# Performance work log

Hardware: AMD Instinct MI355X
Metric: run time of the kernel (lower is better)

The kernel has to match this reference:

```python
import jax, jax.numpy as jnp
import numpy as np
import math

D = 64          # emb_size
R = 32          # num relations
MAX_LEN = 5000  # position table size
E = 30000       # num edges / relation instances
EPSILON = 0.01
THETA = 0.01


def _build_Q():
    # sinusoidal axes [MAX_LEN, D]
    position = jnp.arange(MAX_LEN, dtype=jnp.float32)[:, None]
    div_term = jnp.exp(jnp.arange(0, D, 2, dtype=jnp.float32) * (-math.log(10000.0) / D))
    axes = jnp.zeros((MAX_LEN, D), dtype=jnp.float32)
    axes = axes.at[:, 0::2].set(jnp.sin(position * div_term))
    axes = axes.at[:, 1::2].set(jnp.cos(position * div_term))
    # skew-symmetric generator S_ij = theta * (a_i - a_j); Q = expm(S)  [MAX_LEN, D, D]
    S = THETA * (axes[..., None] - axes[:, None, :])
    Q = jax.scipy.linalg.expm(S)
    return Q


def setup_inputs() -> dict:
    key = jax.random.key(0)
    k1, k2, k3, k4, k5 = jax.random.split(key, 5)
    std = 1.0 / jnp.sqrt(jnp.float32(D))
    relation_embs = jax.random.normal(k1, (R, D, D), dtype=jnp.float32) * std
    Q = _build_Q()
    relation_mapping = jax.random.randint(k2, (E, 2), 0, 2 * R, dtype=jnp.int64 if jax.config.jax_enable_x64 else jnp.int32)
    node_mapping = jax.random.randint(k3, (MAX_LEN,), 0, MAX_LEN)
    edge_index = jax.random.randint(k4, (2, E), 0, MAX_LEN)
    node_embs = jax.random.normal(k5, (MAX_LEN, D), dtype=jnp.float32)
    return {
        "relation_mapping": relation_mapping,
        "node_mapping": node_mapping,
        "edge_index": edge_index,
        "node_embs": node_embs,
        "relation_embs": relation_embs,
        "Q": Q,
    }


def reference(relation_mapping, node_mapping, edge_index, node_embs, relation_embs, Q):
    # node_mapping, edge_index, node_embs are unused by the original forward
    I = jnp.eye(D, dtype=relation_embs.dtype)
    W_even = I + EPSILON * relation_embs   # [R, D, D]
    W_odd = I - EPSILON * relation_embs    # [R, D, D]
    # interleave -> W[2r] = W_even[r], W[2r+1] = W_odd[r]   [2R, D, D]
    W = jnp.stack([W_even, W_odd], axis=1).reshape(-1, D, D)
    Qg = Q[relation_mapping[:, 0]]         # [E, D, D] gather
    rel = W[relation_mapping[:, 1]]        # [E, D, D] gather
    # Q^T @ rel @ Q per edge
    out = jnp.einsum('eji,ejk,ekl->eil', Qg, rel, Qg)
    return out  # dropout p=0.0 is identity
```

## Files before the change

kernel.cpp:

```cpp
#include <hip/hip_runtime.h>

#define TRE_EPS 0.01f
#define TRE_CAP 256
#define TRE_NB  2048

typedef float tre_f4 __attribute__((ext_vector_type(4)));
typedef short tre_bf8 __attribute__((ext_vector_type(8)));

__device__ __forceinline__ unsigned short tre_f2bf(float f) {
    unsigned int u = __float_as_uint(f);
    u += 0x7fffu + ((u >> 16) & 1u);
    return (unsigned short)(u >> 16);
}
__device__ __forceinline__ unsigned long long tre_pack4(float a, float b,
                                                        float c, float d) {
    return (unsigned long long)tre_f2bf(a)
         | ((unsigned long long)tre_f2bf(b) << 16)
         | ((unsigned long long)tre_f2bf(c) << 32)
         | ((unsigned long long)tre_f2bf(d) << 48);
}

__global__ __launch_bounds__(256) void tre_bin(
    const int* __restrict__ rm, int E,
    int* __restrict__ counts, int* __restrict__ list)
{
    int e = blockIdx.x * 256 + threadIdx.x;
    if (e >= E) return;
    int g  = rm[2 * e + 0];
    int r2 = rm[2 * e + 1];
    int b  = (g << 5) | (r2 >> 1);
    int idx = atomicAdd(&counts[b], 1);
    if (idx < TRE_CAP)
        list[b * TRE_CAP + idx] = (e << 1) | (r2 & 1);
}

__global__ __launch_bounds__(256) void tre_pair(
    const float* __restrict__ Q, const float* __restrict__ RE,
    const int* __restrict__ counts, const int* __restrict__ list,
    float* __restrict__ out)
{
    __shared__ __align__(16) unsigned char sB[16384];
    __shared__ int sList[TRE_CAP];

    const int b = blockIdx.x;
    const int g = b >> 5;
    const int r = b & 31;
    const int t = threadIdx.x;
    const int lane = t & 63;
    const int wv = t >> 6;
    const int fr = lane & 15;
    const int fq = lane >> 4;
    const int i0 = wv << 4;

    const int cnt_raw = counts[b];
    const int cnt = cnt_raw > TRE_CAP ? TRE_CAP : cnt_raw;
    if (t < cnt) sList[t] = list[b * TRE_CAP + t];

    const float* Qg  = Q  + ((size_t)g << 12);
    const float* REr = RE + ((size_t)r << 12);

    unsigned char* REb = sB;
    unsigned char* Qtb = sB + 8192;

    for (int i = t; i < 1024; i += 256) {
        float4 w = ((const float4*)REr)[i];
        int R = i >> 4, c0 = (i & 15) << 2;
        int o = c0 * 2;
        *(unsigned long long*)(REb + R * 128 + (o ^ ((R & 7) << 4))) =
            tre_pack4(w.x, w.y, w.z, w.w);
    }
    for (int it = 0; it < 4; ++it) {
        int k0 = (wv << 2) + (it << 4);
        float q0 = Qg[(k0 + 0) * 64 + lane];
        float q1 = Qg[(k0 + 1) * 64 + lane];
        float q2 = Qg[(k0 + 2) * 64 + lane];
        float q3 = Qg[(k0 + 3) * 64 + lane];
        int R = lane, o = k0 * 2;
        *(unsigned long long*)(Qtb + R * 128 + (o ^ ((R & 7) << 4))) =
            tre_pack4(q0, q1, q2, q3);
    }
    __syncthreads();

    tre_f4 accA[4];
#pragma unroll
    for (int jf = 0; jf < 4; ++jf) accA[jf] = (tre_f4){0.f, 0.f, 0.f, 0.f};
#pragma unroll
    for (int ks = 0; ks < 2; ++ks) {
        int ko = ks * 64 + fq * 16;
        int Ra = i0 + fr;
        tre_bf8 afr = *(const tre_bf8*)(REb + Ra * 128 + (ko ^ ((Ra & 7) << 4)));
#pragma unroll
        for (int jf = 0; jf < 4; ++jf) {
            int Rb = (jf << 4) + fr;
            tre_bf8 bfr = *(const tre_bf8*)(Qtb + Rb * 128 + (ko ^ ((Rb & 7) << 4)));
            accA[jf] = __builtin_amdgcn_mfma_f32_16x16x32_bf16(afr, bfr, accA[jf], 0, 0, 0);
        }
    }
    __syncthreads();

#pragma unroll
    for (int jf = 0; jf < 4; ++jf) {
        int C  = (jf << 4) + fr;
        int r0 = i0 + (fq << 2);
        int o  = r0 * 2;
        *(unsigned long long*)(sB + C * 128 + (o ^ ((C & 7) << 4))) =
            tre_pack4(accA[jf][0], accA[jf][1], accA[jf][2], accA[jf][3]);
    }
    __syncthreads();

    tre_f4 accM[4];
#pragma unroll
    for (int jf = 0; jf < 4; ++jf) accM[jf] = (tre_f4){0.f, 0.f, 0.f, 0.f};
#pragma unroll
    for (int ks = 0; ks < 2; ++ks) {
        int ko = ks * 64 + fq * 16;
        int Ra = i0 + fr;
        tre_bf8 afr = *(const tre_bf8*)(Qtb + Ra * 128 + (ko ^ ((Ra & 7) << 4)));
#pragma unroll
        for (int jf = 0; jf < 4; ++jf) {
            int Rb = (jf << 4) + fr;
            tre_bf8 bfr = *(const tre_bf8*)(sB + Rb * 128 + (ko ^ ((Rb & 7) << 4)));
            accM[jf] = __builtin_amdgcn_mfma_f32_16x16x32_bf16(afr, bfr, accM[jf], 0, 0, 0);
        }
    }
    __syncthreads();

    float* sM = (float*)sB;
#pragma unroll
    for (int jf = 0; jf < 4; ++jf) {
        int c  = (jf << 4) + fr;
        int r0 = i0 + (fq << 2);
        sM[(r0 + 0) * 64 + c] = accM[jf][0];
        sM[(r0 + 1) * 64 + c] = accM[jf][1];
        sM[(r0 + 2) * 64 + c] = accM[jf][2];
        sM[(r0 + 3) * 64 + c] = accM[jf][3];
    }
    __syncthreads();

    tre_f4 mreg[4], diag[4];
#pragma unroll
    for (int j = 0; j < 4; ++j) {
        mreg[j] = *(const tre_f4*)&sM[(t + 256 * j) << 2];
        int f = (t + 256 * j) << 2;
#pragma unroll
        for (int c = 0; c < 4; ++c) {
            int fc = f + c;
            diag[j][c] = ((fc >> 6) == (fc & 63)) ? 1.0f : 0.0f;
        }
    }

    if (cnt > 0) {
        int pk = sList[0];
        for (int i = 0; i < cnt; ++i) {
            int nxt = (i + 1 < cnt) ? sList[i + 1] : 0;
            int e = pk >> 1;
            float s = (pk & 1) ? -TRE_EPS : TRE_EPS;
            tre_f4* dst = (tre_f4*)(out + ((size_t)e << 12));
#pragma unroll
            for (int j = 0; j < 4; ++j) {
                tre_f4 v = s * mreg[j] + diag[j];
                __builtin_nontemporal_store(v, &dst[t + 256 * j]);
            }
            pk = nxt;
        }
    }
}

__global__ __launch_bounds__(256) void tre_direct(
    const int* __restrict__ rm, const float* __restrict__ Q,
    const float* __restrict__ RE, float* __restrict__ out)
{
    __shared__ float sQ[64 * 64];
    __shared__ float sW[64 * 65];

    const int e = blockIdx.x;
    const int g  = rm[2 * e + 0];
    const int r2 = rm[2 * e + 1];
    const int r  = r2 >> 1;
    const float s = (r2 & 1) ? -TRE_EPS : TRE_EPS;
    const int t = threadIdx.x;
    const int i0 = (t >> 4) << 2;
    const int l0 = (t & 15) << 2;

    const float* Qg  = Q  + ((size_t)g << 12);
    const float* REr = RE + ((size_t)r << 12);
    for (int i = t; i < 1024; i += 256) {
        ((float4*)sQ)[i] = ((const float4*)Qg)[i];
        float4 w = ((const float4*)REr)[i];
        int row = i >> 4, col = (i & 15) << 2;
        float* dst = &sW[row * 65 + col];
        dst[0] = w.x; dst[1] = w.y; dst[2] = w.z; dst[3] = w.w;
    }
    __syncthreads();

    float a[4][4] = {{0,0,0,0},{0,0,0,0},{0,0,0,0},{0,0,0,0}};
#pragma unroll 8
    for (int k = 0; k < 64; ++k) {
        float4 qv = *(const float4*)&sQ[(k << 6) + l0];
#pragma unroll
        for (int d = 0; d < 4; ++d) {
            float w = sW[(i0 + d) * 65 + k];
            a[d][0] = fmaf(w, qv.x, a[d][0]);
            a[d][1] = fmaf(w, qv.y, a[d][1]);
            a[d][2] = fmaf(w, qv.z, a[d][2]);
            a[d][3] = fmaf(w, qv.w, a[d][3]);
        }
    }
    __syncthreads();
    float* sA = sW;
#pragma unroll
    for (int d = 0; d < 4; ++d)
        *(float4*)&sA[(i0 + d) * 64 + l0] =
            make_float4(a[d][0], a[d][1], a[d][2], a[d][3]);
    __syncthreads();

    float qtq[4][4] = {{0,0,0,0},{0,0,0,0},{0,0,0,0},{0,0,0,0}};
    float qta[4][4] = {{0,0,0,0},{0,0,0,0},{0,0,0,0},{0,0,0,0}};
#pragma unroll 4
    for (int j = 0; j < 64; ++j) {
        float4 qi = *(const float4*)&sQ[(j << 6) + i0];
        float4 ql = *(const float4*)&sQ[(j << 6) + l0];
        float4 av = *(const float4*)&sA[(j << 6) + l0];
        float qiv[4] = {qi.x, qi.y, qi.z, qi.w};
        float qlv[4] = {ql.x, ql.y, ql.z, ql.w};
        float avv[4] = {av.x, av.y, av.z, av.w};
#pragma unroll
        for (int d = 0; d < 4; ++d)
#pragma unroll
            for (int ee = 0; ee < 4; ++ee) {
                qtq[d][ee] = fmaf(qiv[d], qlv[ee], qtq[d][ee]);
                qta[d][ee] = fmaf(qiv[d], avv[ee], qta[d][ee]);
            }
    }
    float* dst = out + ((size_t)e << 12);
#pragma unroll
    for (int d = 0; d < 4; ++d) {
        float4 v;
        v.x = fmaf(s, qta[d][0], qtq[d][0]);
        v.y = fmaf(s, qta[d][1], qtq[d][1]);
        v.z = fmaf(s, qta[d][2], qtq[d][2]);
        v.w = fmaf(s, qta[d][3], qtq[d][3]);
        *(float4*)&dst[(i0 + d) * 64 + l0] = v;
    }
}

extern "C" void kernel_launch(void* const* d_in, const int* in_sizes, int n_in,
                              void* d_out, int out_size, void* d_ws, size_t ws_size,
                              hipStream_t stream) {
    const int*   rm = (const int*)d_in[0];
    const float* RE = (const float*)d_in[4];
    const float* Q  = (const float*)d_in[5];
    float* out = (float*)d_out;
    const int E = in_sizes[0] / 2;

    const size_t cnt_bytes  = (size_t)TRE_NB * sizeof(int);
    const size_t list_bytes = (size_t)TRE_NB * TRE_CAP * sizeof(int);
    const size_t need = cnt_bytes + list_bytes;

    if (ws_size >= need) {
        int* counts = (int*)d_ws;
        int* list   = (int*)((char*)d_ws + cnt_bytes);
        hipMemsetAsync(counts, 0, cnt_bytes, stream);
        hipLaunchKernelGGL(tre_bin, dim3((E + 255) / 256), dim3(256), 0, stream,
                           rm, E, counts, list);
        hipLaunchKernelGGL(tre_pair, dim3(TRE_NB), dim3(256), 0, stream,
                           Q, RE, counts, list, out);
    } else {
        hipLaunchKernelGGL(tre_direct, dim3(E), dim3(256), 0, stream,
                           rm, Q, RE, out);
    }
}
```

Measured before the change: 116.1 us.

## Make pair kernel persistent with atomic work-stealing over bins

Turns the per-bin pair kernel into a persistent kernel launched with a fixed grid. Each block takes further bins from a global atomic cursor, which tre_bin initialises. Empty bins are skipped before any Q/RE loads, and load imbalance from uneven bin counts should even out through dynamic scheduling. In exchange it adds an atomic and two barriers per bin and serialises bins within a block.

```diff
diff --git a/kernel.cpp b/kernel.cpp
--- a/kernel.cpp
+++ b/kernel.cpp
@@ -1,8 +1,9 @@
 #include <hip/hip_runtime.h>
 
-#define TRE_EPS 0.01f
-#define TRE_CAP 256
-#define TRE_NB  2048
+#define TRE_EPS   0.01f
+#define TRE_CAP   256
+#define TRE_NB    2048
+#define TRE_PGRID 1024
 
 typedef float tre_f4 __attribute__((ext_vector_type(4)));
 typedef short tre_bf8 __attribute__((ext_vector_type(8)));
@@ -22,8 +23,9 @@
 
 __global__ __launch_bounds__(256) void tre_bin(
     const int* __restrict__ rm, int E,
-    int* __restrict__ counts, int* __restrict__ list)
+    int* __restrict__ counts, int* __restrict__ list, int* __restrict__ cursor)
 {
+    if (blockIdx.x == 0 && threadIdx.x == 0) *cursor = TRE_PGRID;
     int e = blockIdx.x * 256 + threadIdx.x;
     if (e >= E) return;
     int g  = rm[2 * e + 0];
@@ -34,17 +36,15 @@
         list[b * TRE_CAP + idx] = (e << 1) | (r2 & 1);
 }
 
-__global__ __launch_bounds__(256) void tre_pair(
+__global__ __launch_bounds__(256, 4) void tre_pair(
     const float* __restrict__ Q, const float* __restrict__ RE,
     const int* __restrict__ counts, const int* __restrict__ list,
-    float* __restrict__ out)
+    int* __restrict__ cursor, float* __restrict__ out)
 {
     __shared__ __align__(16) unsigned char sB[16384];
     __shared__ int sList[TRE_CAP];
-
-    const int b = blockIdx.x;
-    const int g = b >> 5;
-    const int r = b & 31;
+    __shared__ int sTicket;
+
     const int t = threadIdx.x;
     const int lane = t & 63;
     const int wv = t >> 6;
@@ -52,95 +52,12 @@
     const int fq = lane >> 4;
     const int i0 = wv << 4;
 
-    const int cnt_raw = counts[b];
-    const int cnt = cnt_raw > TRE_CAP ? TRE_CAP : cnt_raw;
-    if (t < cnt) sList[t] = list[b * TRE_CAP + t];
-
-    const float* Qg  = Q  + ((size_t)g << 12);
-    const float* REr = RE + ((size_t)r << 12);
-
     unsigned char* REb = sB;
     unsigned char* Qtb = sB + 8192;
 
-    for (int i = t; i < 1024; i += 256) {
-        float4 w = ((const float4*)REr)[i];
-        int R = i >> 4, c0 = (i & 15) << 2;
-        int o = c0 * 2;
-        *(unsigned long long*)(REb + R * 128 + (o ^ ((R & 7) << 4))) =
-            tre_pack4(w.x, w.y, w.z, w.w);
-    }
-    for (int it = 0; it < 4; ++it) {
-        int k0 = (wv << 2) + (it << 4);
-        float q0 = Qg[(k0 + 0) * 64 + lane];
-        float q1 = Qg[(k0 + 1) * 64 + lane];
-        float q2 = Qg[(k0 + 2) * 64 + lane];
-        float q3 = Qg[(k0 + 3) * 64 + lane];
-        int R = lane, o = k0 * 2;
-        *(unsigned long long*)(Qtb + R * 128 + (o ^ ((R & 7) << 4))) =
-            tre_pack4(q0, q1, q2, q3);
-    }
-    __syncthreads();
-
-    tre_f4 accA[4];
-#pragma unroll
-    for (int jf = 0; jf < 4; ++jf) accA[jf] = (tre_f4){0.f, 0.f, 0.f, 0.f};
-#pragma unroll
-    for (int ks = 0; ks < 2; ++ks) {
-        int ko = ks * 64 + fq * 16;
-        int Ra = i0 + fr;
-        tre_bf8 afr = *(const tre_bf8*)(REb + Ra * 128 + (ko ^ ((Ra & 7) << 4)));
-#pragma unroll
-        for (int jf = 0; jf < 4; ++jf) {
-            int Rb = (jf << 4) + fr;
-            tre_bf8 bfr = *(const tre_bf8*)(Qtb + Rb * 128 + (ko ^ ((Rb & 7) << 4)));
-            accA[jf] = __builtin_amdgcn_mfma_f32_16x16x32_bf16(afr, bfr, accA[jf], 0, 0, 0);
-        }
-    }
-    __syncthreads();
-
-#pragma unroll
-    for (int jf = 0; jf < 4; ++jf) {
-        int C  = (jf << 4) + fr;
-        int r0 = i0 + (fq << 2);
-        int o  = r0 * 2;
-        *(unsigned long long*)(sB + C * 128 + (o ^ ((C & 7) << 4))) =
-            tre_pack4(accA[jf][0], accA[jf][1], accA[jf][2], accA[jf][3]);
-    }
-    __syncthreads();
-
-    tre_f4 accM[4];
-#pragma unroll
-    for (int jf = 0; jf < 4; ++jf) accM[jf] = (tre_f4){0.f, 0.f, 0.f, 0.f};
-#pragma unroll
-    for (int ks = 0; ks < 2; ++ks) {
-        int ko = ks * 64 + fq * 16;
-        int Ra = i0 + fr;
-        tre_bf8 afr = *(const tre_bf8*)(Qtb + Ra * 128 + (ko ^ ((Ra & 7) << 4)));
-#pragma unroll
-        for (int jf = 0; jf < 4; ++jf) {
-            int Rb = (jf << 4) + fr;
-            tre_bf8 bfr = *(const tre_bf8*)(sB + Rb * 128 + (ko ^ ((Rb & 7) << 4)));
-            accM[jf] = __builtin_amdgcn_mfma_f32_16x16x32_bf16(afr, bfr, accM[jf], 0, 0, 0);
-        }
-    }
-    __syncthreads();
-
-    float* sM = (float*)sB;
-#pragma unroll
-    for (int jf = 0; jf < 4; ++jf) {
-        int c  = (jf << 4) + fr;
-        int r0 = i0 + (fq << 2);
-        sM[(r0 + 0) * 64 + c] = accM[jf][0];
-        sM[(r0 + 1) * 64 + c] = accM[jf][1];
-        sM[(r0 + 2) * 64 + c] = accM[jf][2];
-        sM[(r0 + 3) * 64 + c] = accM[jf][3];
-    }
-    __syncthreads();
-
-    tre_f4 mreg[4], diag[4];
+    tre_f4 diag[4];
 #pragma unroll
     for (int j = 0; j < 4; ++j) {
-        mreg[j] = *(const tre_f4*)&sM[(t + 256 * j) << 2];
         int f = (t + 256 * j) << 2;
 #pragma unroll
         for (int c = 0; c < 4; ++c) {
@@ -149,20 +66,120 @@
         }
     }
 
-    if (cnt > 0) {
-        int pk = sList[0];
-        for (int i = 0; i < cnt; ++i) {
-            int nxt = (i + 1 < cnt) ? sList[i + 1] : 0;
-            int e = pk >> 1;
-            float s = (pk & 1) ? -TRE_EPS : TRE_EPS;
-            tre_f4* dst = (tre_f4*)(out + ((size_t)e << 12));
-#pragma unroll
-            for (int j = 0; j < 4; ++j) {
-                tre_f4 v = s * mreg[j] + diag[j];
-                __builtin_nontemporal_store(v, &dst[t + 256 * j]);
-            }
-            pk = nxt;
+    int b = blockIdx.x;
+    for (;;) {
+        if (b >= TRE_NB) break;
+
+        const int cnt_raw = counts[b];
+        const int cnt = cnt_raw > TRE_CAP ? TRE_CAP : cnt_raw;
+
+        if (cnt > 0) {
+            const int g = b >> 5;
+            const int r = b & 31;
+            const float* Qg  = Q  + ((size_t)g << 12);
+            const float* REr = RE + ((size_t)r << 12);
+
+            if (t < cnt) sList[t] = list[b * TRE_CAP + t];
+
+            for (int i = t; i < 1024; i += 256) {
+                float4 w = ((const float4*)REr)[i];
+                int R = i >> 4, c0 = (i & 15) << 2;
+                int o = c0 * 2;
+                *(unsigned long long*)(REb + R * 128 + (o ^ ((R & 7) << 4))) =
+                    tre_pack4(w.x, w.y, w.z, w.w);
+            }
+            for (int it = 0; it < 4; ++it) {
+                int k0 = (wv << 2) + (it << 4);
+                float q0 = Qg[(k0 + 0) * 64 + lane];
+                float q1 = Qg[(k0 + 1) * 64 + lane];
+                float q2 = Qg[(k0 + 2) * 64 + lane];
+                float q3 = Qg[(k0 + 3) * 64 + lane];
+                int R = lane, o = k0 * 2;
+                *(unsigned long long*)(Qtb + R * 128 + (o ^ ((R & 7) << 4))) =
+                    tre_pack4(q0, q1, q2, q3);
+            }
+            __syncthreads();
+
+            tre_f4 accA[4];
+#pragma unroll
+            for (int jf = 0; jf < 4; ++jf) accA[jf] = (tre_f4){0.f, 0.f, 0.f, 0.f};
+#pragma unroll
+            for (int ks = 0; ks < 2; ++ks) {
+                int ko = ks * 64 + fq * 16;
+                int Ra = i0 + fr;
+                tre_bf8 afr = *(const tre_bf8*)(REb + Ra * 128 + (ko ^ ((Ra & 7) << 4)));
+#pragma unroll
+                for (int jf = 0; jf < 4; ++jf) {
+                    int Rb = (jf << 4) + fr;
+                    tre_bf8 bfr = *(const tre_bf8*)(Qtb + Rb * 128 + (ko ^ ((Rb & 7) << 4)));
+                    accA[jf] = __builtin_amdgcn_mfma_f32_16x16x32_bf16(afr, bfr, accA[jf], 0, 0, 0);
+                }
+            }
+            __syncthreads();
+
+#pragma unroll
+            for (int jf = 0; jf < 4; ++jf) {
+                int C  = (jf << 4) + fr;
+                int r0 = i0 + (fq << 2);
+                int o  = r0 * 2;
+                *(unsigned long long*)(sB + C * 128 + (o ^ ((C & 7) << 4))) =
+                    tre_pack4(accA[jf][0], accA[jf][1], accA[jf][2], accA[jf][3]);
+            }
+            __syncthreads();
+
+            tre_f4 accM[4];
+#pragma unroll
+            for (int jf = 0; jf < 4; ++jf) accM[jf] = (tre_f4){0.f, 0.f, 0.f, 0.f};
+#pragma unroll
+            for (int ks = 0; ks < 2; ++ks) {
+                int ko = ks * 64 + fq * 16;
+                int Ra = i0 + fr;
+                tre_bf8 afr = *(const tre_bf8*)(Qtb + Ra * 128 + (ko ^ ((Ra & 7) << 4)));
+#pragma unroll
+                for (int jf = 0; jf < 4; ++jf) {
+                    int Rb = (jf << 4) + fr;
+                    tre_bf8 bfr = *(const tre_bf8*)(sB + Rb * 128 + (ko ^ ((Rb & 7) << 4)));
+                    accM[jf] = __builtin_amdgcn_mfma_f32_16x16x32_bf16(afr, bfr, accM[jf], 0, 0, 0);
+                }
+            }
+            __syncthreads();
+
+            float* sM = (float*)sB;
+#pragma unroll
+            for (int jf = 0; jf < 4; ++jf) {
+                int cc = (jf << 4) + fr;
+                int r0 = i0 + (fq << 2);
+                sM[(r0 + 0) * 64 + cc] = accM[jf][0];
+                sM[(r0 + 1) * 64 + cc] = accM[jf][1];
+                sM[(r0 + 2) * 64 + cc] = accM[jf][2];
+                sM[(r0 + 3) * 64 + cc] = accM[jf][3];
+            }
+            __syncthreads();
+
+            tre_f4 mreg[4];
+#pragma unroll
+            for (int j = 0; j < 4; ++j)
+                mreg[j] = *(const tre_f4*)&sM[(t + 256 * j) << 2];
+
+            int pk = sList[0];
+            for (int i = 0; i < cnt; ++i) {
+                int nxt = (i + 1 < cnt) ? sList[i + 1] : 0;
+                int e = pk >> 1;
+                float s = (pk & 1) ? -TRE_EPS : TRE_EPS;
+                tre_f4* dst = (tre_f4*)(out + ((size_t)e << 12));
+#pragma unroll
+                for (int j = 0; j < 4; ++j) {
+                    tre_f4 v = s * mreg[j] + diag[j];
+                    __builtin_nontemporal_store(v, &dst[t + 256 * j]);
+                }
+                pk = nxt;
+            }
         }
+
+        __syncthreads();
+        if (t == 0) sTicket = atomicAdd(cursor, 1);
+        __syncthreads();
+        b = sTicket;
     }
 }
 
@@ -254,17 +271,19 @@
     const int E = in_sizes[0] / 2;
 
     const size_t cnt_bytes  = (size_t)TRE_NB * sizeof(int);
+    const size_t cur_bytes  = 16;
     const size_t list_bytes = (size_t)TRE_NB * TRE_CAP * sizeof(int);
-    const size_t need = cnt_bytes + list_bytes;
+    const size_t need = cnt_bytes + cur_bytes + list_bytes;
 
     if (ws_size >= need) {
         int* counts = (int*)d_ws;
-        int* list   = (int*)((char*)d_ws + cnt_bytes);
-        hipMemsetAsync(counts, 0, cnt_bytes, stream);
+        int* cursor = (int*)((char*)d_ws + cnt_bytes);
+        int* list   = (int*)((char*)d_ws + cnt_bytes + cur_bytes);
+        hipMemsetAsync(counts, 0, cnt_bytes + cur_bytes, stream);
         hipLaunchKernelGGL(tre_bin, dim3((E + 255) / 256), dim3(256), 0, stream,
-                           rm, E, counts, list);
-        hipLaunchKernelGGL(tre_pair, dim3(TRE_NB), dim3(256), 0, stream,
-                           Q, RE, counts, list, out);
+                           rm, E, counts, list, cursor);
+        hipLaunchKernelGGL(tre_pair, dim3(TRE_PGRID), dim3(256), 0, stream,
+                           Q, RE, counts, list, cursor, out);
     } else {
         hipLaunchKernelGGL(tre_direct, dim3(E), dim3(256), 0, stream,
                            rm, Q, RE, out);
```

After: 111.8 us. 3.6% less time.

## Precompute per-(Q,relation) tiles in bf16 workspace, then stream one block per edge

Applied to the files above, without the earlier changes.

The atomic binning pass and the per-bin edge loop are removed. A build kernel now computes the 2048 distinct Q^T·R·Q products and stores them as bf16 tiles in the workspace. A second kernel launches one block per edge, reads its tile, applies ±eps scaling plus identity, and streams the fp32 output. This removes the memset, the atomics and the uneven per-bin work, at the cost of a 16MB intermediate write and about 8KB of tile reads per edge, which should mostly hit cache.

```diff
diff --git a/kernel.cpp b/kernel.cpp
--- a/kernel.cpp
+++ b/kernel.cpp
@@ -1,16 +1,19 @@
 #include <hip/hip_runtime.h>
 
 #define TRE_EPS 0.01f
-#define TRE_CAP 256
 #define TRE_NB  2048
 
 typedef float tre_f4 __attribute__((ext_vector_type(4)));
 typedef short tre_bf8 __attribute__((ext_vector_type(8)));
+typedef unsigned short tre_us8 __attribute__((ext_vector_type(8)));
 
 __device__ __forceinline__ unsigned short tre_f2bf(float f) {
     unsigned int u = __float_as_uint(f);
     u += 0x7fffu + ((u >> 16) & 1u);
     return (unsigned short)(u >> 16);
+}
+__device__ __forceinline__ float tre_bf2f(unsigned short u) {
+    return __uint_as_float(((unsigned int)u) << 16);
 }
 __device__ __forceinline__ unsigned long long tre_pack4(float a, float b,
                                                         float c, float d) {
@@ -20,27 +23,11 @@
          | ((unsigned long long)tre_f2bf(d) << 48);
 }
 
-__global__ __launch_bounds__(256) void tre_bin(
-    const int* __restrict__ rm, int E,
-    int* __restrict__ counts, int* __restrict__ list)
-{
-    int e = blockIdx.x * 256 + threadIdx.x;
-    if (e >= E) return;
-    int g  = rm[2 * e + 0];
-    int r2 = rm[2 * e + 1];
-    int b  = (g << 5) | (r2 >> 1);
-    int idx = atomicAdd(&counts[b], 1);
-    if (idx < TRE_CAP)
-        list[b * TRE_CAP + idx] = (e << 1) | (r2 & 1);
-}
-
-__global__ __launch_bounds__(256) void tre_pair(
+__global__ __launch_bounds__(256) void tre_build(
     const float* __restrict__ Q, const float* __restrict__ RE,
-    const int* __restrict__ counts, const int* __restrict__ list,
-    float* __restrict__ out)
+    unsigned short* __restrict__ Tm)
 {
     __shared__ __align__(16) unsigned char sB[16384];
-    __shared__ int sList[TRE_CAP];
 
     const int b = blockIdx.x;
     const int g = b >> 5;
@@ -52,13 +39,8 @@
     const int fq = lane >> 4;
     const int i0 = wv << 4;
 
-    const int cnt_raw = counts[b];
-    const int cnt = cnt_raw > TRE_CAP ? TRE_CAP : cnt_raw;
-    if (t < cnt) sList[t] = list[b * TRE_CAP + t];
-
     const float* Qg  = Q  + ((size_t)g << 12);
     const float* REr = RE + ((size_t)r << 12);
-
     unsigned char* REb = sB;
     unsigned char* Qtb = sB + 8192;
 
@@ -128,41 +110,51 @@
     float* sM = (float*)sB;
 #pragma unroll
     for (int jf = 0; jf < 4; ++jf) {
-        int c  = (jf << 4) + fr;
+        int cc = (jf << 4) + fr;
         int r0 = i0 + (fq << 2);
-        sM[(r0 + 0) * 64 + c] = accM[jf][0];
-        sM[(r0 + 1) * 64 + c] = accM[jf][1];
-        sM[(r0 + 2) * 64 + c] = accM[jf][2];
-        sM[(r0 + 3) * 64 + c] = accM[jf][3];
-    }
-    __syncthreads();
-
-    tre_f4 mreg[4], diag[4];
+        sM[(r0 + 0) * 64 + cc] = accM[jf][0];
+        sM[(r0 + 1) * 64 + cc] = accM[jf][1];
+        sM[(r0 + 2) * 64 + cc] = accM[jf][2];
+        sM[(r0 + 3) * 64 + cc] = accM[jf][3];
+    }
+    __syncthreads();
+
+    unsigned short* dst = Tm + ((size_t)b << 12);
+#pragma unroll
+    for (int jj = 0; jj < 2; ++jj) {
+        int u = t + 256 * jj;
+        const float* src = &sM[u << 3];
+        tre_us8 p;
+#pragma unroll
+        for (int c = 0; c < 8; ++c) p[c] = tre_f2bf(src[c]);
+        *(tre_us8*)(dst + (u << 3)) = p;
+    }
+}
+
+__global__ __launch_bounds__(256) void tre_edge(
+    const int* __restrict__ rm, const unsigned short* __restrict__ Tm,
+    float* __restrict__ out)
+{
+    const int e  = blockIdx.x;
+    const int g  = rm[2 * e + 0];
+    const int r2 = rm[2 * e + 1];
+    const float s = (r2 & 1) ? -TRE_EPS : TRE_EPS;
+
+    const ushort4* tile = (const ushort4*)(Tm + (((size_t)((g << 5) | (r2 >> 1))) << 12));
+    tre_f4* dst = (tre_f4*)(out + ((size_t)e << 12));
+    const int t = threadIdx.x;
+
 #pragma unroll
     for (int j = 0; j < 4; ++j) {
-        mreg[j] = *(const tre_f4*)&sM[(t + 256 * j) << 2];
-        int f = (t + 256 * j) << 2;
-#pragma unroll
-        for (int c = 0; c < 4; ++c) {
-            int fc = f + c;
-            diag[j][c] = ((fc >> 6) == (fc & 63)) ? 1.0f : 0.0f;
-        }
-    }
-
-    if (cnt > 0) {
-        int pk = sList[0];
-        for (int i = 0; i < cnt; ++i) {
-            int nxt = (i + 1 < cnt) ? sList[i + 1] : 0;
-            int e = pk >> 1;
-            float s = (pk & 1) ? -TRE_EPS : TRE_EPS;
-            tre_f4* dst = (tre_f4*)(out + ((size_t)e << 12));
-#pragma unroll
-            for (int j = 0; j < 4; ++j) {
-                tre_f4 v = s * mreg[j] + diag[j];
-                __builtin_nontemporal_store(v, &dst[t + 256 * j]);
-            }
-            pk = nxt;
-        }
+        int u = t + 256 * j;
+        ushort4 m4 = tile[u];
+        int f = u << 2;
+        tre_f4 v;
+        v.x = fmaf(s, tre_bf2f(m4.x), (((f + 0) >> 6) == ((f + 0) & 63)) ? 1.0f : 0.0f);
+        v.y = fmaf(s, tre_bf2f(m4.y), (((f + 1) >> 6) == ((f + 1) & 63)) ? 1.0f : 0.0f);
+        v.z = fmaf(s, tre_bf2f(m4.z), (((f + 2) >> 6) == ((f + 2) & 63)) ? 1.0f : 0.0f);
+        v.w = fmaf(s, tre_bf2f(m4.w), (((f + 3) >> 6) == ((f + 3) & 63)) ? 1.0f : 0.0f);
+        __builtin_nontemporal_store(v, &dst[u]);
     }
 }
 
@@ -253,18 +245,14 @@
     float* out = (float*)d_out;
     const int E = in_sizes[0] / 2;
 
-    const size_t cnt_bytes  = (size_t)TRE_NB * sizeof(int);
-    const size_t list_bytes = (size_t)TRE_NB * TRE_CAP * sizeof(int);
-    const size_t need = cnt_bytes + list_bytes;
-
-    if (ws_size >= need) {
-        int* counts = (int*)d_ws;
-        int* list   = (int*)((char*)d_ws + cnt_bytes);
-        hipMemsetAsync(counts, 0, cnt_bytes, stream);
-        hipLaunchKernelGGL(tre_bin, dim3((E + 255) / 256), dim3(256), 0, stream,
-                           rm, E, counts, list);
-        hipLaunchKernelGGL(tre_pair, dim3(TRE_NB), dim3(256), 0, stream,
-                           Q, RE, counts, list, out);
+    const size_t tm_bytes = (size_t)TRE_NB * 4096 * sizeof(unsigned short);
+
+    if (ws_size >= tm_bytes) {
+        unsigned short* Tm = (unsigned short*)d_ws;
+        hipLaunchKernelGGL(tre_build, dim3(TRE_NB), dim3(256), 0, stream,
+                           Q, RE, Tm);
+        hipLaunchKernelGGL(tre_edge, dim3(E), dim3(256), 0, stream,
+                           rm, Tm, out);
     } else {
         hipLaunchKernelGGL(tre_direct, dim3(E), dim3(256), 0, stream,
                            rm, Q, RE, out);
```

After: 117.5 us. Within noise of the previous version (+1.2%).
